# Kernel optimization log

Hardware: AMD Instinct MI355X
Metric: run time of the kernel (lower is better)

## Reference

```python
import jax, jax.numpy as jnp
import numpy as np

GAMMA = 267.513e6  # gyromagnetic ratio of 1H, rad/s/T


def setup_inputs() -> dict:
    key = jax.random.key(0)
    k1, k2 = jax.random.split(key, 2)
    N_meas = 64
    g = jax.random.normal(k2, (N_meas, 3), dtype=jnp.float32)
    g = g / jnp.linalg.norm(g, axis=1, keepdims=True)          # unit gradient directions
    G_amps = 0.02 + 0.06 * jax.random.uniform(k1, (N_meas,), dtype=jnp.float32)  # 20-80 mT/m
    return {
        "G_amps": G_amps,
        "gradients": g,
        "D_long": jnp.float32(2.0e-9),    # m^2/s, fiber-parallel diffusivity
        "D_trans": jnp.float32(5.0e-10),  # m^2/s, transverse diffusivity
        "delta_us": 10000,  # gradient pulse duration, microseconds
        "Delta_us": 30000,  # pulse separation, microseconds
        "dt_us": 100,       # SDE step, microseconds
        "N_particles": 50000,
        "seed": 0,
    }


def reference(G_amps, gradients, D_long, D_trans, delta_us, Delta_us, dt_us, N_particles, seed):
    dt = dt_us * 1e-6
    delta = delta_us * 1e-6
    Delta = Delta_us * 1e-6
    T_max = Delta + delta + dt
    times = jnp.arange(0.0, T_max, dt, dtype=jnp.float32)      # (T,)
    T = times.shape[0]

    # --- Euler-Maruyama SDE solve (free anisotropic diffusion, fiber = e_z, k_conf=0) ---
    # per-axis noise scale: sqrt(2 * D * dt), transverse on x/y, longitudinal on z
    sig = jnp.sqrt(2.0 * dt * jnp.stack([D_trans, D_trans, D_long]))  # (3,)
    base_key = jax.random.key(seed)
    y0 = jnp.zeros((N_particles, 3), dtype=jnp.float32)

    def step(y, i):
        n = jax.random.normal(jax.random.fold_in(base_key, i), (N_particles, 3), dtype=jnp.float32)
        y_next = y + sig * n
        return y_next, y_next

    _, rest = jax.lax.scan(step, y0, jnp.arange(T - 1))
    traj = jnp.concatenate([y0[None], rest], axis=0)           # (T, N, 3)

    # --- trapezoidal PGSE gradient envelope (rise time = dt), shared across measurements ---
    rise = dt
    def pulse(t0):
        return (jnp.clip((times - t0) / rise, 0.0, 1.0)
                - jnp.clip((times - t0 - delta) / rise, 0.0, 1.0))
    env = pulse(0.0) - pulse(Delta)                            # (T,)

    # --- phase integration, fused: contract time first to avoid (M,T,N) intermediates ---
    S = jnp.einsum('t,tnd->nd', env, traj)                     # (N, 3) envelope-weighted position sum
    phases = (GAMMA * dt) * jnp.einsum('m,md,nd->mn', G_amps, gradients, S)  # (M, N)
    c = jnp.mean(jnp.cos(phases), axis=1)
    s = jnp.mean(jnp.sin(phases), axis=1)
    return jnp.sqrt(c * c + s * s)                             # |mean exp(i*phase)| per measurement
```

## Files before the change

kernel.cpp:

```cpp
#include <hip/hip_runtime.h>
#include <stdint.h>

#define N_PART  50000
#define HALF_N  25000
#define STEPS   400
#define T_PTS   401
#define CHUNKS  20
#define SPC     (STEPS / CHUNKS)
#define BITS_SPLIT 75000u
#define NSPLIT  8

__device__ __forceinline__ void threefry2x32(uint32_t k0, uint32_t k1,
                                             uint32_t x0, uint32_t x1,
                                             uint32_t& o0, uint32_t& o1) {
  const uint32_t ks2 = k0 ^ k1 ^ 0x1BD11BDAu;
  x0 += k0; x1 += k1;
#define RND(r) { x0 += x1; x1 = (x1 << r) | (x1 >> (32 - r)); x1 ^= x0; }
  RND(13) RND(15) RND(26) RND(6)
  x0 += k1;  x1 += ks2 + 1u;
  RND(17) RND(29) RND(16) RND(24)
  x0 += ks2; x1 += k0 + 2u;
  RND(13) RND(15) RND(26) RND(6)
  x0 += k0;  x1 += k1 + 3u;
  RND(17) RND(29) RND(16) RND(24)
  x0 += k1;  x1 += ks2 + 4u;
  RND(13) RND(15) RND(26) RND(6)
  x0 += ks2; x1 += k0 + 5u;
#undef RND
  o0 = x0; o1 = x1;
}

__device__ __forceinline__ float bits_to_erfinv(uint32_t bits) {
  const float lo = __uint_as_float(0xBF7FFFFFu);
  float m = __uint_as_float((bits >> 9) | 0x3F800000u);
  float u = fmaxf(lo, fmaf(m, 2.0f, -3.0f));
  float t = fmaf(-u, u, 1.0f);
  float L = __log2f(t);
  float p;
  if (L > -7.2134752f) {
    float w = fmaf(L, -0.69314718056f, -2.5f);
    p = 2.81022636e-08f;
    p = fmaf(p, w, 3.43273939e-07f);
    p = fmaf(p, w, -3.5233877e-06f);
    p = fmaf(p, w, -4.39150654e-06f);
    p = fmaf(p, w, 0.00021858087f);
    p = fmaf(p, w, -0.00125372503f);
    p = fmaf(p, w, -0.00417768164f);
    p = fmaf(p, w, 0.246640727f);
    p = fmaf(p, w, 1.50140941f);
  } else {
    float w = sqrtf(L * -0.69314718056f) - 3.0f;
    p = -0.000200214257f;
    p = fmaf(p, w, 0.000100950558f);
    p = fmaf(p, w, 0.00134934322f);
    p = fmaf(p, w, -0.00367342844f);
    p = fmaf(p, w, 0.00573950773f);
    p = fmaf(p, w, -0.0076224613f);
    p = fmaf(p, w, 0.00943887047f);
    p = fmaf(p, w, 1.00167406f);
    p = fmaf(p, w, 2.83297682f);
  }
  return p * u;
}

__global__ __launch_bounds__(512) void setup_kernel(
    const int* __restrict__ delta_us, const int* __restrict__ Delta_us,
    const int* __restrict__ dt_us, const int* __restrict__ seed,
    uint4* __restrict__ kw, float* __restrict__ Sbuf, float* __restrict__ acc) {
  __shared__ float env_s[T_PTS];
  int tid = threadIdx.x;

  if (blockIdx.x == 0) {
    if (tid < T_PTS) {
      float u  = (float)dt_us[0]    * 1e-6f;
      float df = (float)delta_us[0] * 1e-6f;
      float Df = (float)Delta_us[0] * 1e-6f;
      float tm = (float)tid * u;
      float c1 = fminf(fmaxf(tm / u, 0.0f), 1.0f);
      float c2 = fminf(fmaxf((tm - df) / u, 0.0f), 1.0f);
      float c3 = fminf(fmaxf((tm - Df) / u, 0.0f), 1.0f);
      float c4 = fminf(fmaxf(((tm - Df) - df) / u, 0.0f), 1.0f);
      env_s[tid] = (c1 - c2) - (c3 - c4);
    }
    __syncthreads();
    if (tid < STEPS) {
      float w = 0.0f;
      for (int t = tid + 1; t < T_PTS; ++t) w += env_s[t];
      uint32_t o0, o1;
      threefry2x32(0u, (uint32_t)seed[0], 0u, (uint32_t)tid, o0, o1);
      kw[tid] = make_uint4(o0, o1, __float_as_uint(1.41421356237309515f * w), 0u);
    }
  }
  for (int i = blockIdx.x * blockDim.x + tid; i < N_PART * 3; i += gridDim.x * blockDim.x)
    Sbuf[i] = 0.0f;
  if (blockIdx.x == 1 && tid < 132) acc[tid] = 0.0f;
}

__global__ __launch_bounds__(256) void sde_kernel(const uint4* __restrict__ kw,
                                                  const float* __restrict__ D_long,
                                                  const float* __restrict__ D_trans,
                                                  const int* __restrict__ dt_us,
                                                  float* __restrict__ Sbuf) {
  uint32_t tid = blockIdx.x * 256 + threadIdx.x;
  uint32_t chunk = tid / HALF_N;
  uint32_t p = tid - chunk * HALF_N;
  if (chunk >= CHUNKS) return;
  const uint32_t c0 = 3u * p;
  const int i0 = (int)chunk * SPC;

  float a0x = 0.f, a0y = 0.f, a0z = 0.f;
  float a1x = 0.f, a1y = 0.f, a1z = 0.f;

  for (int s = 0; s < SPC; ++s) {
    uint4 k = kw[i0 + s];
    float w = __uint_as_float(k.z);
    uint32_t o0, o1;
    threefry2x32(k.x, k.y, c0,      c0 + BITS_SPLIT,      o0, o1);
    a0x = fmaf(w, bits_to_erfinv(o0), a0x);
    a1x = fmaf(w, bits_to_erfinv(o1), a1x);
    threefry2x32(k.x, k.y, c0 + 1u, c0 + 1u + BITS_SPLIT, o0, o1);
    a0y = fmaf(w, bits_to_erfinv(o0), a0y);
    a1y = fmaf(w, bits_to_erfinv(o1), a1y);
    threefry2x32(k.x, k.y, c0 + 2u, c0 + 2u + BITS_SPLIT, o0, o1);
    a0z = fmaf(w, bits_to_erfinv(o0), a0z);
    a1z = fmaf(w, bits_to_erfinv(o1), a1z);
  }

  float twodt = 2.0f * ((float)dt_us[0] * 1e-6f);
  float st = sqrtf(twodt * D_trans[0]);
  float sl = sqrtf(twodt * D_long[0]);

  atomicAdd(&Sbuf[3 * p + 0], a0x * st);
  atomicAdd(&Sbuf[3 * p + 1], a0y * st);
  atomicAdd(&Sbuf[3 * p + 2], a0z * sl);
  atomicAdd(&Sbuf[3 * (p + HALF_N) + 0], a1x * st);
  atomicAdd(&Sbuf[3 * (p + HALF_N) + 1], a1y * st);
  atomicAdd(&Sbuf[3 * (p + HALF_N) + 2], a1z * sl);
}

__global__ __launch_bounds__(256) void signal_partial(const float* __restrict__ Sbuf,
                                                      const float* __restrict__ G_amps,
                                                      const float* __restrict__ grad,
                                                      const int* __restrict__ dt_us,
                                                      float* __restrict__ acc,
                                                      float* __restrict__ out) {
  int m = blockIdx.x;
  int n0 = blockIdx.y * (N_PART / NSPLIT);
  int tid = threadIdx.x;
  float Kf = 267.513e6f * ((float)dt_us[0] * 1e-6f);
  float Km = Kf * G_amps[m];
  float gx = grad[3 * m + 0], gy = grad[3 * m + 1], gz = grad[3 * m + 2];

  float cs = 0.f, ss = 0.f;
  for (int n = n0 + tid; n < n0 + N_PART / NSPLIT; n += 256) {
    float sx = Sbuf[3 * n + 0], sy = Sbuf[3 * n + 1], sz = Sbuf[3 * n + 2];
    float ph = Km * (gx * sx + gy * sy + gz * sz);
    float s, c;
    __sincosf(ph, &s, &c);
    cs += c; ss += s;
  }
  for (int off = 32; off > 0; off >>= 1) {
    cs += __shfl_down(cs, off);
    ss += __shfl_down(ss, off);
  }
  __shared__ float redc[4], reds[4];
  __shared__ int slast;
  int lane = tid & 63, wv = tid >> 6;
  if (lane == 0) { redc[wv] = cs; reds[wv] = ss; }
  __syncthreads();
  if (tid == 0) {
    atomicAdd(&acc[m],      redc[0] + redc[1] + redc[2] + redc[3]);
    atomicAdd(&acc[64 + m], reds[0] + reds[1] + reds[2] + reds[3]);
    __threadfence();
    unsigned* ctr = (unsigned*)&acc[128];
    unsigned done = __hip_atomic_fetch_add(ctr, 1u, __ATOMIC_ACQ_REL, __HIP_MEMORY_SCOPE_AGENT);
    slast = (done == (unsigned)(gridDim.x * gridDim.y) - 1u) ? 1 : 0;
  }
  __syncthreads();
  if (slast && tid < (int)gridDim.x) {
    float c = __hip_atomic_load(&acc[tid],      __ATOMIC_RELAXED, __HIP_MEMORY_SCOPE_AGENT) / (float)N_PART;
    float s = __hip_atomic_load(&acc[64 + tid], __ATOMIC_RELAXED, __HIP_MEMORY_SCOPE_AGENT) / (float)N_PART;
    out[tid] = sqrtf(c * c + s * s);
  }
}

extern "C" void kernel_launch(void* const* d_in, const int* in_sizes, int n_in,
                              void* d_out, int out_size, void* d_ws, size_t ws_size,
                              hipStream_t stream) {
  const float* G_amps   = (const float*)d_in[0];
  const float* grad     = (const float*)d_in[1];
  const float* D_long   = (const float*)d_in[2];
  const float* D_trans  = (const float*)d_in[3];
  const int*   delta_us = (const int*)d_in[4];
  const int*   Delta_us = (const int*)d_in[5];
  const int*   dt_us    = (const int*)d_in[6];
  const int*   seed     = (const int*)d_in[8];

  uint4* kw   = (uint4*)d_ws;
  float* Sbuf = (float*)((char*)d_ws + 6400);
  float* acc  = (float*)((char*)d_ws + 6400 + 600000);

  setup_kernel<<<294, 512, 0, stream>>>(delta_us, Delta_us, dt_us, seed, kw, Sbuf, acc);
  int sde_blocks = (CHUNKS * HALF_N + 255) / 256;
  sde_kernel<<<sde_blocks, 256, 0, stream>>>(kw, D_long, D_trans, dt_us, Sbuf);
  int M = in_sizes[0];
  signal_partial<<<dim3(M, NSPLIT), 256, 0, stream>>>(Sbuf, G_amps, grad, dt_us, acc, (float*)d_out);
}
```

Measured before the change: 186.3 us.

## Fuse setup, SDE and signal kernels into one persistent kernel with grid barriers

Merges the three kernels into one persistent kernel of 977 blocks. Each block recomputes the per-step keys and weights into shared memory, runs the SDE accumulation over two passes, then passes two software grid barriers before the phase/sincos reduction and the final output. Zeroing moves to a hipMemsetAsync. This removes launch gaps and the global kw table, at the cost of redundant per-block setup work and spin barriers that need every block resident at once (about 4 blocks per CU).

```diff
diff --git a/kernel.cpp b/kernel.cpp
--- a/kernel.cpp
+++ b/kernel.cpp
@@ -8,7 +8,10 @@
 #define CHUNKS  20
 #define SPC     (STEPS / CHUNKS)
 #define BITS_SPLIT 75000u
-#define NSPLIT  8
+#define GRID    977
+#define BLK     256
+#define NSPLIT  15
+#define TILE_P  3334
 
 __device__ __forceinline__ void threefry2x32(uint32_t k0, uint32_t k1,
                                              uint32_t x0, uint32_t x1,
@@ -63,123 +66,135 @@
   return p * u;
 }
 
-__global__ __launch_bounds__(512) void setup_kernel(
+__device__ __forceinline__ void grid_barrier(unsigned* ctr, int tid) {
+  __syncthreads();
+  if (tid == 0) {
+    __threadfence();
+    __hip_atomic_fetch_add(ctr, 1u, __ATOMIC_RELEASE, __HIP_MEMORY_SCOPE_AGENT);
+    int guard = 0;
+    while (__hip_atomic_load(ctr, __ATOMIC_ACQUIRE, __HIP_MEMORY_SCOPE_AGENT) < (unsigned)GRID
+           && ++guard < 300000000) {
+      __builtin_amdgcn_s_sleep(2);
+    }
+  }
+  __syncthreads();
+}
+
+__global__ __launch_bounds__(BLK, 4) void fused_kernel(
+    const float* __restrict__ G_amps, const float* __restrict__ grad,
+    const float* __restrict__ D_long, const float* __restrict__ D_trans,
     const int* __restrict__ delta_us, const int* __restrict__ Delta_us,
     const int* __restrict__ dt_us, const int* __restrict__ seed,
-    uint4* __restrict__ kw, float* __restrict__ Sbuf, float* __restrict__ acc) {
+    float* __restrict__ Sbuf, float* __restrict__ acc, unsigned* __restrict__ ctr,
+    float* __restrict__ out, int M) {
+
   __shared__ float env_s[T_PTS];
+  __shared__ uint32_t K0ls[STEPS], K1ls[STEPS];
+  __shared__ float Wls[STEPS];
   int tid = threadIdx.x;
 
-  if (blockIdx.x == 0) {
-    if (tid < T_PTS) {
-      float u  = (float)dt_us[0]    * 1e-6f;
-      float df = (float)delta_us[0] * 1e-6f;
-      float Df = (float)Delta_us[0] * 1e-6f;
-      float tm = (float)tid * u;
+  {
+    float u  = (float)dt_us[0]    * 1e-6f;
+    float df = (float)delta_us[0] * 1e-6f;
+    float Df = (float)Delta_us[0] * 1e-6f;
+    for (int t = tid; t < T_PTS; t += BLK) {
+      float tm = (float)t * u;
       float c1 = fminf(fmaxf(tm / u, 0.0f), 1.0f);
       float c2 = fminf(fmaxf((tm - df) / u, 0.0f), 1.0f);
       float c3 = fminf(fmaxf((tm - Df) / u, 0.0f), 1.0f);
       float c4 = fminf(fmaxf(((tm - Df) - df) / u, 0.0f), 1.0f);
-      env_s[tid] = (c1 - c2) - (c3 - c4);
+      env_s[t] = (c1 - c2) - (c3 - c4);
     }
     __syncthreads();
-    if (tid < STEPS) {
+    for (int i = tid; i < STEPS; i += BLK) {
       float w = 0.0f;
-      for (int t = tid + 1; t < T_PTS; ++t) w += env_s[t];
+      for (int t = i + 1; t < T_PTS; ++t) w += env_s[t];
       uint32_t o0, o1;
-      threefry2x32(0u, (uint32_t)seed[0], 0u, (uint32_t)tid, o0, o1);
-      kw[tid] = make_uint4(o0, o1, __float_as_uint(1.41421356237309515f * w), 0u);
-    }
-  }
-  for (int i = blockIdx.x * blockDim.x + tid; i < N_PART * 3; i += gridDim.x * blockDim.x)
-    Sbuf[i] = 0.0f;
-  if (blockIdx.x == 1 && tid < 132) acc[tid] = 0.0f;
-}
-
-__global__ __launch_bounds__(256) void sde_kernel(const uint4* __restrict__ kw,
-                                                  const float* __restrict__ D_long,
-                                                  const float* __restrict__ D_trans,
-                                                  const int* __restrict__ dt_us,
-                                                  float* __restrict__ Sbuf) {
-  uint32_t tid = blockIdx.x * 256 + threadIdx.x;
-  uint32_t chunk = tid / HALF_N;
-  uint32_t p = tid - chunk * HALF_N;
-  if (chunk >= CHUNKS) return;
-  const uint32_t c0 = 3u * p;
-  const int i0 = (int)chunk * SPC;
-
-  float a0x = 0.f, a0y = 0.f, a0z = 0.f;
-  float a1x = 0.f, a1y = 0.f, a1z = 0.f;
-
-  for (int s = 0; s < SPC; ++s) {
-    uint4 k = kw[i0 + s];
-    float w = __uint_as_float(k.z);
-    uint32_t o0, o1;
-    threefry2x32(k.x, k.y, c0,      c0 + BITS_SPLIT,      o0, o1);
-    a0x = fmaf(w, bits_to_erfinv(o0), a0x);
-    a1x = fmaf(w, bits_to_erfinv(o1), a1x);
-    threefry2x32(k.x, k.y, c0 + 1u, c0 + 1u + BITS_SPLIT, o0, o1);
-    a0y = fmaf(w, bits_to_erfinv(o0), a0y);
-    a1y = fmaf(w, bits_to_erfinv(o1), a1y);
-    threefry2x32(k.x, k.y, c0 + 2u, c0 + 2u + BITS_SPLIT, o0, o1);
-    a0z = fmaf(w, bits_to_erfinv(o0), a0z);
-    a1z = fmaf(w, bits_to_erfinv(o1), a1z);
-  }
-
-  float twodt = 2.0f * ((float)dt_us[0] * 1e-6f);
-  float st = sqrtf(twodt * D_trans[0]);
-  float sl = sqrtf(twodt * D_long[0]);
-
-  atomicAdd(&Sbuf[3 * p + 0], a0x * st);
-  atomicAdd(&Sbuf[3 * p + 1], a0y * st);
-  atomicAdd(&Sbuf[3 * p + 2], a0z * sl);
-  atomicAdd(&Sbuf[3 * (p + HALF_N) + 0], a1x * st);
-  atomicAdd(&Sbuf[3 * (p + HALF_N) + 1], a1y * st);
-  atomicAdd(&Sbuf[3 * (p + HALF_N) + 2], a1z * sl);
-}
-
-__global__ __launch_bounds__(256) void signal_partial(const float* __restrict__ Sbuf,
-                                                      const float* __restrict__ G_amps,
-                                                      const float* __restrict__ grad,
-                                                      const int* __restrict__ dt_us,
-                                                      float* __restrict__ acc,
-                                                      float* __restrict__ out) {
-  int m = blockIdx.x;
-  int n0 = blockIdx.y * (N_PART / NSPLIT);
-  int tid = threadIdx.x;
-  float Kf = 267.513e6f * ((float)dt_us[0] * 1e-6f);
-  float Km = Kf * G_amps[m];
-  float gx = grad[3 * m + 0], gy = grad[3 * m + 1], gz = grad[3 * m + 2];
-
-  float cs = 0.f, ss = 0.f;
-  for (int n = n0 + tid; n < n0 + N_PART / NSPLIT; n += 256) {
-    float sx = Sbuf[3 * n + 0], sy = Sbuf[3 * n + 1], sz = Sbuf[3 * n + 2];
-    float ph = Km * (gx * sx + gy * sy + gz * sz);
-    float s, c;
-    __sincosf(ph, &s, &c);
-    cs += c; ss += s;
-  }
-  for (int off = 32; off > 0; off >>= 1) {
-    cs += __shfl_down(cs, off);
-    ss += __shfl_down(ss, off);
-  }
-  __shared__ float redc[4], reds[4];
-  __shared__ int slast;
-  int lane = tid & 63, wv = tid >> 6;
-  if (lane == 0) { redc[wv] = cs; reds[wv] = ss; }
-  __syncthreads();
-  if (tid == 0) {
-    atomicAdd(&acc[m],      redc[0] + redc[1] + redc[2] + redc[3]);
-    atomicAdd(&acc[64 + m], reds[0] + reds[1] + reds[2] + reds[3]);
-    __threadfence();
-    unsigned* ctr = (unsigned*)&acc[128];
-    unsigned done = __hip_atomic_fetch_add(ctr, 1u, __ATOMIC_ACQ_REL, __HIP_MEMORY_SCOPE_AGENT);
-    slast = (done == (unsigned)(gridDim.x * gridDim.y) - 1u) ? 1 : 0;
-  }
-  __syncthreads();
-  if (slast && tid < (int)gridDim.x) {
-    float c = __hip_atomic_load(&acc[tid],      __ATOMIC_RELAXED, __HIP_MEMORY_SCOPE_AGENT) / (float)N_PART;
-    float s = __hip_atomic_load(&acc[64 + tid], __ATOMIC_RELAXED, __HIP_MEMORY_SCOPE_AGENT) / (float)N_PART;
+      threefry2x32(0u, (uint32_t)seed[0], 0u, (uint32_t)i, o0, o1);
+      K0ls[i] = o0; K1ls[i] = o1;
+      Wls[i] = 1.41421356237309515f * w;
+    }
+    __syncthreads();
+  }
+
+  {
+    float twodt = 2.0f * ((float)dt_us[0] * 1e-6f);
+    float st = sqrtf(twodt * D_trans[0]);
+    float sl = sqrtf(twodt * D_long[0]);
+    uint32_t T = blockIdx.x * BLK + tid;
+    for (int pass = 0; pass < 2; ++pass) {
+      uint32_t item = T + (uint32_t)pass * (GRID * BLK);
+      if (item < CHUNKS * HALF_N) {
+        uint32_t chunk = item / HALF_N;
+        uint32_t p = item - chunk * HALF_N;
+        const uint32_t c0 = 3u * p;
+        const int i0 = (int)chunk * SPC;
+        float a0x = 0.f, a0y = 0.f, a0z = 0.f;
+        float a1x = 0.f, a1y = 0.f, a1z = 0.f;
+        for (int s = 0; s < SPC; ++s) {
+          uint32_t k0 = K0ls[i0 + s], k1 = K1ls[i0 + s];
+          float w = Wls[i0 + s];
+          uint32_t o0, o1;
+          threefry2x32(k0, k1, c0,      c0 + BITS_SPLIT,      o0, o1);
+          a0x = fmaf(w, bits_to_erfinv(o0), a0x);
+          a1x = fmaf(w, bits_to_erfinv(o1), a1x);
+          threefry2x32(k0, k1, c0 + 1u, c0 + 1u + BITS_SPLIT, o0, o1);
+          a0y = fmaf(w, bits_to_erfinv(o0), a0y);
+          a1y = fmaf(w, bits_to_erfinv(o1), a1y);
+          threefry2x32(k0, k1, c0 + 2u, c0 + 2u + BITS_SPLIT, o0, o1);
+          a0z = fmaf(w, bits_to_erfinv(o0), a0z);
+          a1z = fmaf(w, bits_to_erfinv(o1), a1z);
+        }
+        atomicAdd(&Sbuf[3 * p + 0], a0x * st);
+        atomicAdd(&Sbuf[3 * p + 1], a0y * st);
+        atomicAdd(&Sbuf[3 * p + 2], a0z * sl);
+        atomicAdd(&Sbuf[3 * (p + HALF_N) + 0], a1x * st);
+        atomicAdd(&Sbuf[3 * (p + HALF_N) + 1], a1y * st);
+        atomicAdd(&Sbuf[3 * (p + HALF_N) + 2], a1z * sl);
+      }
+    }
+  }
+
+  grid_barrier(&ctr[0], tid);
+
+  {
+    int tile = blockIdx.x;
+    if (tile < M * NSPLIT) {
+      int m = tile % 64;
+      int splitIdx = tile / 64;
+      int n0 = splitIdx * TILE_P;
+      int n1 = n0 + TILE_P; if (n1 > N_PART) n1 = N_PART;
+      float Kf = 267.513e6f * ((float)dt_us[0] * 1e-6f);
+      float Km = Kf * G_amps[m];
+      float gx = grad[3 * m + 0], gy = grad[3 * m + 1], gz = grad[3 * m + 2];
+      float cs = 0.f, ss = 0.f;
+      for (int n = n0 + tid; n < n1; n += BLK) {
+        float sx = Sbuf[3 * n + 0], sy = Sbuf[3 * n + 1], sz = Sbuf[3 * n + 2];
+        float ph = Km * (gx * sx + gy * sy + gz * sz);
+        float s, c;
+        __sincosf(ph, &s, &c);
+        cs += c; ss += s;
+      }
+      for (int off = 32; off > 0; off >>= 1) {
+        cs += __shfl_down(cs, off);
+        ss += __shfl_down(ss, off);
+      }
+      __shared__ float redc[4], reds[4];
+      int lane = tid & 63, wv = tid >> 6;
+      if (lane == 0) { redc[wv] = cs; reds[wv] = ss; }
+      __syncthreads();
+      if (tid == 0) {
+        atomicAdd(&acc[m],      redc[0] + redc[1] + redc[2] + redc[3]);
+        atomicAdd(&acc[64 + m], reds[0] + reds[1] + reds[2] + reds[3]);
+      }
+    }
+  }
+
+  grid_barrier(&ctr[1], tid);
+
+  if (blockIdx.x == 0 && tid < M) {
+    float c = acc[tid]      / (float)N_PART;
+    float s = acc[64 + tid] / (float)N_PART;
     out[tid] = sqrtf(c * c + s * s);
   }
 }
@@ -196,13 +211,13 @@
   const int*   dt_us    = (const int*)d_in[6];
   const int*   seed     = (const int*)d_in[8];
 
-  uint4* kw   = (uint4*)d_ws;
-  float* Sbuf = (float*)((char*)d_ws + 6400);
-  float* acc  = (float*)((char*)d_ws + 6400 + 600000);
-
-  setup_kernel<<<294, 512, 0, stream>>>(delta_us, Delta_us, dt_us, seed, kw, Sbuf, acc);
-  int sde_blocks = (CHUNKS * HALF_N + 255) / 256;
-  sde_kernel<<<sde_blocks, 256, 0, stream>>>(kw, D_long, D_trans, dt_us, Sbuf);
+  float*    Sbuf = (float*)d_ws;
+  float*    acc  = (float*)((char*)d_ws + 600000);
+  unsigned* ctr  = (unsigned*)((char*)d_ws + 600512);
+
+  hipMemsetAsync(d_ws, 0, 600520, stream);
   int M = in_sizes[0];
-  signal_partial<<<dim3(M, NSPLIT), 256, 0, stream>>>(Sbuf, G_amps, grad, dt_us, acc, (float*)d_out);
-}
+  fused_kernel<<<GRID, BLK, 0, stream>>>(G_amps, grad, D_long, D_trans,
+                                         delta_us, Delta_us, dt_us, seed,
+                                         Sbuf, acc, ctr, (float*)d_out, M);
+}
```

Result: slower. 395.1 us (+112.1%).
